# Performance work log

Measured on AMD Instinct MI355X. Metric: run time of the kernel, lower is better.

Reference implementation:

```python
import jax, jax.numpy as jnp
import numpy as np

B, Q, N, E, D, H, EDIM = 64, 50, 32, 64, 128, 4, 8
NEG = -1e30

def _ln(x, g, b, eps=1e-5):
    mu = x.mean(-1, keepdims=True)
    var = ((x - mu) ** 2).mean(-1, keepdims=True)
    return (x - mu) / jnp.sqrt(var + eps) * g + b

def setup_inputs():
    key = jax.random.key(0)
    ks = jax.random.split(key, 12)
    s = 1.0 / np.sqrt(D)
    return {
        "query_embeddings": jax.random.normal(ks[0], (B, Q, N, D), jnp.float32),
        "query_maskings": jnp.ones((B, Q, N), jnp.int32),
        "edge_indexes": jax.random.randint(ks[1], (B, Q, 2, E), 0, N, dtype=jnp.int32),
        "edge_weights": jax.random.randint(ks[2], (B, Q, E), 0, 2, dtype=jnp.int32),
        "edge_maskings": jnp.ones((B, Q, E), jnp.int32),
        "ln1_g": jnp.ones((D,), jnp.float32),
        "ln1_b": jnp.zeros((D,), jnp.float32),
        "emb_table": jax.random.normal(ks[3], (2, EDIM), jnp.float32),
        "Wl": jax.random.normal(ks[4], (D, H * D), jnp.float32) * s,
        "bl": jnp.zeros((H * D,), jnp.float32),
        "Wr": jax.random.normal(ks[5], (D, H * D), jnp.float32) * s,
        "br": jnp.zeros((H * D,), jnp.float32),
        "We": jax.random.normal(ks[6], (EDIM, H * D), jnp.float32) / np.sqrt(EDIM),
        "att": jax.random.normal(ks[7], (H, D), jnp.float32) * s,
        "gat_b": jnp.zeros((D,), jnp.float32),
        "W1": jax.random.normal(ks[8], (D, D), jnp.float32) * s,
        "b1": jnp.zeros((D,), jnp.float32),
        "W2": jax.random.normal(ks[9], (D, D), jnp.float32) * s,
        "b2": jnp.zeros((D,), jnp.float32),
        "ln2_g": jnp.ones((D,), jnp.float32),
        "ln2_b": jnp.zeros((D,), jnp.float32),
    }

def _gat_graph(x, src, dst, eemb, emask, Wl, bl, Wr, br, We, att, gat_b):
    # GATv2Conv, heads=H, concat=False, add_self_loops=True (fill_value='mean')
    # x [N,D]; src,dst [E]; eemb [E,EDIM]; emask [E] float
    xl = (x @ Wl + bl).reshape(N, H, D)
    xr = (x @ Wr + br).reshape(N, H, D)
    # self-loop edge_attr = mean of incoming (valid) edge attrs per target node
    ecnt = jax.ops.segment_sum(emask, dst, num_segments=N)
    loop_attr = jax.ops.segment_sum(eemb * emask[:, None], dst, num_segments=N) / jnp.maximum(ecnt, 1.0)[:, None]
    e = (eemb @ We).reshape(E, H, D)
    le = (loop_attr @ We).reshape(N, H, D)
    z = jax.nn.leaky_relu(xl[src] + xr[dst] + e, 0.2)
    logits = jnp.where(emask[:, None] > 0, jnp.einsum('ehd,hd->eh', z, att), NEG)
    zs = jax.nn.leaky_relu(xl + xr + le, 0.2)  # self-loop terms
    logits_s = jnp.einsum('nhd,hd->nh', zs, att)
    # segment softmax over incoming edges + self loop
    m = jnp.maximum(jax.ops.segment_max(logits, dst, num_segments=N), logits_s)  # [N,H]
    exp_e = jnp.where(emask[:, None] > 0, jnp.exp(logits - m[dst]), 0.0)
    exp_s = jnp.exp(logits_s - m)
    denom = jax.ops.segment_sum(exp_e, dst, num_segments=N) + exp_s
    agg = jax.ops.segment_sum(xl[src] * (exp_e / denom[dst])[:, :, None], dst, num_segments=N)
    agg = agg + xl * (exp_s / denom)[:, :, None]
    return agg.mean(axis=1) + gat_b  # concat=False -> mean over heads, + bias

def _forward(query_embeddings, ln1_g, ln1_b, emb_table, Wl, bl, Wr, br, We, att, gat_b,
             W1, b1, W2, b2, ln2_g, ln2_b,
             query_maskings, edge_indexes, edge_weights, edge_maskings):
    x = _ln(query_embeddings, ln1_g, ln1_b)                 # [B,Q,N,D]
    nmask = query_maskings.astype(jnp.float32)              # [B,Q,N]
    emask = edge_maskings.astype(jnp.float32)               # [B,Q,E]
    valid = ((query_maskings.sum(-1) > 0) & (edge_maskings.sum(-1) > 0)).astype(jnp.float32)  # [B,Q]
    eemb = emb_table[edge_weights]                          # [B,Q,E,EDIM]
    G = B * Q
    xf = x.reshape(G, N, D)
    srcf = edge_indexes[:, :, 0, :].reshape(G, E)
    dstf = edge_indexes[:, :, 1, :].reshape(G, E)
    eembf = eemb.reshape(G, E, EDIM)
    emaskf = emask.reshape(G, E)
    gat = jax.vmap(_gat_graph, in_axes=(0, 0, 0, 0, 0) + (None,) * 7)
    gout = gat(xf, srcf, dstf, eembf, emaskf, Wl, bl, Wr, br, We, att, gat_b)  # [G,N,D]
    h = jax.nn.leaky_relu(gout @ W1 + b1, 0.01) @ W2 + b2   # FFN (dropout = eval no-op)
    nmf = nmask.reshape(G, N)
    pooled = (h * nmf[:, :, None]).sum(1) / jnp.maximum(nmf.sum(1), 1.0)[:, None]  # global mean pool
    res = pooled.reshape(B, Q, D) * valid[:, :, None]       # invalid queries stay zero
    return _ln(res, ln2_g, ln2_b)

def reference(query_embeddings, query_maskings, edge_indexes, edge_weights, edge_maskings,
              ln1_g, ln1_b, emb_table, Wl, bl, Wr, br, We, att, gat_b,
              W1, b1, W2, b2, ln2_g, ln2_b):
    return _forward(query_embeddings, ln1_g, ln1_b, emb_table, Wl, bl, Wr, br, We, att, gat_b,
                    W1, b1, W2, b2, ln2_g, ln2_b,
                    query_maskings, edge_indexes, edge_weights, edge_maskings)
```

## Files before the change

### kernel.cpp

```cpp
#include <hip/hip_runtime.h>
#include <math.h>

#define B_ 64
#define Q_ 50
#define N_ 32
#define E_ 64
#define D_ 128
#define H_ 4
#define EDIM_ 8
#define G_ (B_*Q_)

#define WLP_OFF 0
#define WRP_OFF 131072
#define W1P_OFF 262144
#define W2P_OFF 294912
#define EW_OFF  327680

typedef __attribute__((ext_vector_type(8))) short short8;
typedef __attribute__((ext_vector_type(4))) float f32x4;
typedef __attribute__((ext_vector_type(4))) unsigned uint4e;
typedef __attribute__((ext_vector_type(2))) unsigned uint2e;
typedef __attribute__((ext_vector_type(2))) _Float16 half2e;
typedef __attribute__((ext_vector_type(2))) __fp16 fp16v2;
typedef unsigned short ushort_t;
typedef unsigned long long u64;

__device__ __forceinline__ int boff(int r, int d) {
  return (r << 7) + ((d & 0x78) ^ ((r & 7) << 3)) + (d & 7);
}

__device__ __forceinline__ ushort_t f2b(float f) {
  unsigned u = __float_as_uint(f);
  u += 0x7fffu + ((u >> 16) & 1u);
  return (ushort_t)(u >> 16);
}
__device__ __forceinline__ float b2f(ushort_t u) {
  return __uint_as_float(((unsigned)u) << 16);
}
__device__ __forceinline__ unsigned cvtpk(float lo, float hi) {
  unsigned r;
  asm("v_cvt_pk_bf16_f32 %0, %1, %2" : "=v"(r) : "v"(lo), "v"(hi));
  return r;
}
__device__ __forceinline__ unsigned pkrtz(float lo, float hi) {
  union { fp16v2 h; unsigned u; } x;
  x.h = __builtin_amdgcn_cvt_pkrtz(lo, hi);
  return x.u;
}
__device__ __forceinline__ half2e u2h(unsigned u) {
  union { unsigned u; half2e h; } x; x.u = u; return x.h;
}
__device__ __forceinline__ float leakyf(float v, float s) {
  return fmaxf(v, s * v);
}
__device__ __forceinline__ void syncb() {
  asm volatile("s_waitcnt lgkmcnt(0)" ::: "memory");
  __builtin_amdgcn_s_barrier();
  asm volatile("" ::: "memory");
}

__global__ __launch_bounds__(256)
void pack_weights(const float* __restrict__ Wl, const float* __restrict__ Wr,
                  const float* __restrict__ W1, const float* __restrict__ W2,
                  const float* __restrict__ embT, const float* __restrict__ We,
                  unsigned char* __restrict__ ws)
{
  const int i = blockIdx.x * 256 + threadIdx.x;
  ushort_t* wlp = (ushort_t*)(ws + WLP_OFF);
  ushort_t* wrp = (ushort_t*)(ws + WRP_OFF);
  ushort_t* w1p = (ushort_t*)(ws + W1P_OFF);
  ushort_t* w2p = (ushort_t*)(ws + W2P_OFF);
  float* ew = (float*)(ws + EW_OFF);
  if (i < 65536) {
    const int kk = i & 31, n = (i >> 5) & 127, q = (i >> 12) & 3, h = i >> 14;
    wlp[i] = f2b(Wl[(q * 32 + kk) * (H_ * D_) + h * D_ + n]);
    wrp[i] = f2b(Wr[(q * 32 + kk) * (H_ * D_) + h * D_ + n]);
  } else if (i < 65536 + 16384) {
    const int j = i - 65536;
    const int kk = j & 31, n = (j >> 5) & 127, q = j >> 12;
    w1p[j] = f2b(W1[(q * 32 + kk) * D_ + n]);
    w2p[j] = f2b(W2[(q * 32 + kk) * D_ + n]);
  } else if (i < 65536 + 16384 + 1024) {
    const int j = i - 65536 - 16384;
    const int w = j >> 9, hd = j & 511;
    float a = 0.f;
#pragma unroll
    for (int k = 0; k < EDIM_; ++k) a = fmaf(embT[w * EDIM_ + k], We[k * (H_ * D_) + hd], a);
    ew[j] = a;
  }
}

template <bool F16OUT, bool LEAKY>
__device__ __forceinline__ void gemm_e(const short8 aF[2][4], const ushort_t* __restrict__ Bp,
                                       const float* __restrict__ bias, float slope,
                                       ushort_t* __restrict__ dst, int lane, int nq)
{
#pragma unroll
  for (int nt = 0; nt < 2; ++nt) {
    const int colw = nq * 32 + nt * 16 + (lane & 15);
    const int oc0 = nq * 32 + nt * 16 + ((lane >> 4) << 2);
    const float4 bb = *(const float4*)&bias[oc0];
    f32x4 acc0 = {0.f, 0.f, 0.f, 0.f}, acc1 = {0.f, 0.f, 0.f, 0.f};
#pragma unroll
    for (int q = 0; q < 4; ++q) {
      const short8 b = *(const short8*)&Bp[((q << 7) + colw) * 32 + ((lane >> 4) << 3)];
      acc0 = __builtin_amdgcn_mfma_f32_16x16x32_bf16(b, aF[0][q], acc0, 0, 0, 0);
      acc1 = __builtin_amdgcn_mfma_f32_16x16x32_bf16(b, aF[1][q], acc1, 0, 0, 0);
    }
#pragma unroll
    for (int cc = 0; cc < 2; ++cc) {
      const f32x4 a = cc ? acc1 : acc0;
      const int node = cc * 16 + (lane & 15);
      float v0 = a[0] + bb.x, v1 = a[1] + bb.y, v2 = a[2] + bb.z, v3 = a[3] + bb.w;
      if (LEAKY) {
        v0 = leakyf(v0, slope); v1 = leakyf(v1, slope);
        v2 = leakyf(v2, slope); v3 = leakyf(v3, slope);
      }
      uint2e o;
      if (F16OUT) {
        o.x = pkrtz(v0, v1);
        o.y = pkrtz(v2, v3);
      } else {
        o.x = cvtpk(v0, v1);
        o.y = cvtpk(v2, v3);
      }
      *(uint2e*)&dst[boff(node, oc0)] = o;
    }
  }
}

__global__ __launch_bounds__(256, 4)
void gat_main(const unsigned char* __restrict__ ws,
              const float* __restrict__ qe,
              const float* __restrict__ ln1g, const float* __restrict__ ln1b,
              const int* __restrict__ qmask, const int* __restrict__ eidx,
              const int* __restrict__ ewt, const int* __restrict__ emsk,
              const float* __restrict__ bl, const float* __restrict__ br,
              const float* __restrict__ att, const float* __restrict__ gatb,
              const float* __restrict__ b1, const float* __restrict__ b2,
              const float* __restrict__ ln2g, const float* __restrict__ ln2b,
              float* __restrict__ out)
{
  const int g = blockIdx.x, t = threadIdx.x;
  const int lane = t & 63, wave = t >> 6;

  __shared__ __align__(16) ushort_t sX[N_ * D_];
  __shared__ __align__(16) ushort_t sXl[N_ * D_];
  __shared__ __align__(16) ushort_t sXr[N_ * D_];
  __shared__ u64 sInc[N_];
  __shared__ int sSrc[E_], sDst[E_], sWt[E_];
  __shared__ float sEm[E_], sNm[N_], sC0[N_], sC1[N_];
  __shared__ float sValid, sNmSum;

  ushort_t* sEW  = sX;
  ushort_t* sAtt = sX + 1024;
  float* sExpE = (float*)(sX + 1536);
  float* sExpS = (float*)(sX + 1664);
  float* sPool = (float*)(sX + 1728);

  const ushort_t* wlp = (const ushort_t*)(ws + WLP_OFF);
  const ushort_t* wrp = (const ushort_t*)(ws + WRP_OFF);
  const ushort_t* w1p = (const ushort_t*)(ws + W1P_OFF);
  const ushort_t* w2p = (const ushort_t*)(ws + W2P_OFF);

  {
    const int r = t >> 3, d0 = (t & 7) << 4;
    const f32x4* src4 = (const f32x4*)(qe + ((size_t)g * N_ + r) * D_ + d0);
    f32x4 v4[4];
#pragma unroll
    for (int p = 0; p < 4; ++p) v4[p] = __builtin_nontemporal_load(src4 + p);
    const float* v = (const float*)v4;
    float s = 0.f, ss = 0.f;
#pragma unroll
    for (int i = 0; i < 16; ++i) { float x = v[i]; s += x; ss += x * x; }
#pragma unroll
    for (int m = 1; m < 8; m <<= 1) { s += __shfl_xor(s, m); ss += __shfl_xor(ss, m); }
    const float mu = s * (1.f / 128.f);
    const float inv = rsqrtf(ss * (1.f / 128.f) - mu * mu + 1e-5f);
    const f32x4* gg = (const f32x4*)&ln1g[d0];
    const f32x4* bb = (const f32x4*)&ln1b[d0];
    float o[16];
#pragma unroll
    for (int p = 0; p < 4; ++p) {
      const f32x4 g4 = gg[p], b4 = bb[p];
#pragma unroll
      for (int k = 0; k < 4; ++k)
        o[p * 4 + k] = (v[p * 4 + k] - mu) * inv * g4[k] + b4[k];
    }
    uint4e w0, w1;
    w0.x = cvtpk(o[0], o[1]);  w0.y = cvtpk(o[2], o[3]);
    w0.z = cvtpk(o[4], o[5]);  w0.w = cvtpk(o[6], o[7]);
    w1.x = cvtpk(o[8], o[9]);  w1.y = cvtpk(o[10], o[11]);
    w1.z = cvtpk(o[12], o[13]); w1.w = cvtpk(o[14], o[15]);
    *(uint4e*)&sX[boff(r, d0)] = w0;
    *(uint4e*)&sX[boff(r, d0 + 8)] = w1;
  }
  if (t < E_) {
    sSrc[t] = eidx[(size_t)g * 2 * E_ + t];
    sDst[t] = eidx[(size_t)g * 2 * E_ + E_ + t];
    sWt[t] = ewt[(size_t)g * E_ + t];
    sEm[t] = (float)emsk[(size_t)g * E_ + t];
  } else if (t < 96) {
    sNm[t - 64] = (float)qmask[(size_t)g * N_ + (t - 64)];
  }
  syncb();

  short8 aF[2][4];
#pragma unroll
  for (int c = 0; c < 2; ++c)
#pragma unroll
    for (int q = 0; q < 4; ++q)
      aF[c][q] = *(const short8*)&sX[boff(c * 16 + (lane & 15), q * 32 + ((lane >> 4) << 3))];

  {
    const int dl = sDst[lane];
    const float eml = sEm[lane];
    const int wtl = sWt[lane];
    const bool val = eml > 0.f;
    const u64 wt0m = __ballot(wtl == 0);
#pragma unroll
    for (int k = 0; k < 8; ++k) {
      const int n = wave * 8 + k;
      const u64 inc = __ballot(val && dl == n);
      if (lane == k) {
        sInc[n] = inc;
        const float cnt = (float)__popcll(inc);
        const float c0 = (float)__popcll(inc & wt0m);
        const float rinv = 1.f / fmaxf(cnt, 1.f);
        sC0[n] = c0 * rinv;
        sC1[n] = (cnt - c0) * rinv;
      }
    }
    if (wave == 3) {
      float nmv = (lane < 32) ? sNm[lane] : 0.f;
      float emv = eml;
#pragma unroll
      for (int m = 1; m < 64; m <<= 1) { nmv += __shfl_xor(nmv, m); emv += __shfl_xor(emv, m); }
      if (lane == 0) {
        sNmSum = nmv;
        sValid = (nmv > 0.f && emv > 0.f) ? 1.f : 0.f;
      }
    }
  }
  syncb();

  {
    const float* ewg = (const float*)(ws + EW_OFF);
    const f32x4 e4 = *(const f32x4*)&ewg[t << 2];
    uint2e p;
    p.x = pkrtz(e4[0], e4[1]);
    p.y = pkrtz(e4[2], e4[3]);
    *(uint2e*)&sEW[t << 2] = p;
    if (t < 128) {
      const f32x4 a4 = *(const f32x4*)&att[t << 2];
      uint2e q;
      q.x = pkrtz(a4[0], a4[1]);
      q.y = pkrtz(a4[2], a4[3]);
      *(uint2e*)&sAtt[t << 2] = q;
    }
  }

  const half2e pslope = {(_Float16)0.2f, (_Float16)0.2f};
  half2e accA[4] = {}, accB[4] = {};

  for (int h = 0; h < H_; ++h) {
    gemm_e<true, false>(aF, wlp + h * 16384, bl + h * D_, 0.f, sXl, lane, wave);
    gemm_e<true, false>(aF, wrp + h * 16384, br + h * D_, 0.f, sXr, lane, wave);
    syncb();
    {
      const int e = t >> 2, qu = t & 3;
      const int sn = sSrc[e], dn = sDst[e];
      const int ewb = (sWt[e] << 9) + (h << 7);
      float dx = 0.f, dy = 0.f;
#pragma unroll
      for (int ch = 0; ch < 4; ++ch) {
        const int dd = qu * 32 + ch * 8;
        const uint4e xlu = *(const uint4e*)&sXl[boff(sn, dd)];
        const uint4e xru = *(const uint4e*)&sXr[boff(dn, dd)];
        const uint4e ewu = *(const uint4e*)&sEW[ewb + dd];
        const uint4e atu = *(const uint4e*)&sAtt[(h << 7) + dd];
#pragma unroll
        for (int k = 0; k < 4; ++k) {
          half2e z = u2h(xlu[k]) + u2h(xru[k]) + u2h(ewu[k]);
          z = __builtin_elementwise_max(z, z * pslope);
          if (k & 1) dy = __builtin_amdgcn_fdot2(z, u2h(atu[k]), dy, false);
          else       dx = __builtin_amdgcn_fdot2(z, u2h(atu[k]), dx, false);
        }
      }
      float dot = dx + dy;
      dot += __shfl_xor(dot, 1);
      dot += __shfl_xor(dot, 2);
      const float ex = (sEm[e] > 0.f) ? __expf(dot) : 0.f;
      if (qu == 0) sExpE[e] = ex;
    }
    {
      const int n = t >> 3, l8 = t & 7;
      const half2e c02 = {(_Float16)sC0[n], (_Float16)sC0[n]};
      const half2e c12 = {(_Float16)sC1[n], (_Float16)sC1[n]};
      float dx = 0.f, dy = 0.f;
#pragma unroll
      for (int ch = 0; ch < 2; ++ch) {
        const int dd = (l8 << 4) + ch * 8;
        const uint4e xlu = *(const uint4e*)&sXl[boff(n, dd)];
        const uint4e xru = *(const uint4e*)&sXr[boff(n, dd)];
        const uint4e e0u = *(const uint4e*)&sEW[(h << 7) + dd];
        const uint4e e1u = *(const uint4e*)&sEW[512 + (h << 7) + dd];
        const uint4e atu = *(const uint4e*)&sAtt[(h << 7) + dd];
#pragma unroll
        for (int k = 0; k < 4; ++k) {
          half2e lw = u2h(e0u[k]) * c02 + u2h(e1u[k]) * c12;
          half2e z = u2h(xlu[k]) + u2h(xru[k]) + lw;
          z = __builtin_elementwise_max(z, z * pslope);
          if (k & 1) dy = __builtin_amdgcn_fdot2(z, u2h(atu[k]), dy, false);
          else       dx = __builtin_amdgcn_fdot2(z, u2h(atu[k]), dx, false);
        }
      }
      float dot = dx + dy;
      dot += __shfl_xor(dot, 1);
      dot += __shfl_xor(dot, 2);
      dot += __shfl_xor(dot, 4);
      if (l8 == 0) sExpS[n] = __expf(dot);
    }
    syncb();
    {
      const int n = t >> 3, l8 = t & 7, db = l8 << 4;
      const float es = sExpS[n];
      const u64 mb = sInc[n];
      float den = es;
      u64 m2 = mb;
      while (m2) { const int e = __builtin_ctzll(m2); m2 &= m2 - 1; den += sExpE[e]; }
      const float rd = 0.25f / den;
      m2 = mb;
      while (m2) {
        const int e = __builtin_ctzll(m2); m2 &= m2 - 1;
        const _Float16 wh = (_Float16)(rd * sExpE[e]);
        const half2e w2 = {wh, wh};
        const int sn = sSrc[e];
        const uint4e a0 = *(const uint4e*)&sXl[boff(sn, db)];
        const uint4e a1 = *(const uint4e*)&sXl[boff(sn, db + 8)];
#pragma unroll
        for (int k = 0; k < 4; ++k) {
          accA[k] = u2h(a0[k]) * w2 + accA[k];
          accB[k] = u2h(a1[k]) * w2 + accB[k];
        }
      }
      const _Float16 wsh = (_Float16)(rd * es);
      const half2e ws2 = {wsh, wsh};
      const uint4e s0 = *(const uint4e*)&sXl[boff(n, db)];
      const uint4e s1 = *(const uint4e*)&sXl[boff(n, db + 8)];
#pragma unroll
      for (int k = 0; k < 4; ++k) {
        accA[k] = u2h(s0[k]) * ws2 + accA[k];
        accB[k] = u2h(s1[k]) * ws2 + accB[k];
      }
    }
    syncb();
  }

  {
    const int n = t >> 3, l8 = t & 7, db = l8 << 4;
    const float4 g0 = *(const float4*)&gatb[db];
    const float4 g1 = *(const float4*)&gatb[db + 4];
    const float4 g2 = *(const float4*)&gatb[db + 8];
    const float4 g3 = *(const float4*)&gatb[db + 12];
    const float gv[16] = {g0.x, g0.y, g0.z, g0.w, g1.x, g1.y, g1.z, g1.w,
                          g2.x, g2.y, g2.z, g2.w, g3.x, g3.y, g3.z, g3.w};
    uint4e o0, o1;
    unsigned* po0 = (unsigned*)&o0;
    unsigned* po1 = (unsigned*)&o1;
#pragma unroll
    for (int k = 0; k < 4; ++k) {
      po0[k] = cvtpk((float)accA[k].x + gv[2 * k], (float)accA[k].y + gv[2 * k + 1]);
      po1[k] = cvtpk((float)accB[k].x + gv[8 + 2 * k], (float)accB[k].y + gv[8 + 2 * k + 1]);
    }
    *(uint4e*)&sX[boff(n, db)] = o0;
    *(uint4e*)&sX[boff(n, db + 8)] = o1;
  }
  syncb();

  {
    short8 aG[2][4];
#pragma unroll
    for (int c = 0; c < 2; ++c)
#pragma unroll
      for (int q = 0; q < 4; ++q)
        aG[c][q] = *(const short8*)&sX[boff(c * 16 + (lane & 15), q * 32 + ((lane >> 4) << 3))];
    gemm_e<false, true>(aG, w1p, b1, 0.01f, sXl, lane, wave);
    syncb();
#pragma unroll
    for (int c = 0; c < 2; ++c)
#pragma unroll
      for (int q = 0; q < 4; ++q)
        aG[c][q] = *(const short8*)&sXl[boff(c * 16 + (lane & 15), q * 32 + ((lane >> 4) << 3))];
    gemm_e<false, false>(aG, w2p, b2, 0.f, sXr, lane, wave);
  }
  syncb();

  if (t < D_) {
    float acc = 0.f;
    for (int n = 0; n < N_; ++n) acc = fmaf(b2f(sXr[boff(n, t)]), sNm[n], acc);
    sPool[t] = acc * (1.f / fmaxf(sNmSum, 1.f)) * sValid;
  }
  syncb();
  if (t < 64) {
    const float v0 = sPool[t], v1 = sPool[t + 64];
    float s = v0 + v1, ss = v0 * v0 + v1 * v1;
#pragma unroll
    for (int m = 1; m < 64; m <<= 1) { s += __shfl_xor(s, m); ss += __shfl_xor(ss, m); }
    const float mu = s * (1.f / 128.f);
    const float inv = rsqrtf(ss * (1.f / 128.f) - mu * mu + 1e-5f);
    float* op = out + (size_t)g * D_;
    __builtin_nontemporal_store((v0 - mu) * inv * ln2g[t] + ln2b[t], op + t);
    __builtin_nontemporal_store((v1 - mu) * inv * ln2g[t + 64] + ln2b[t + 64], op + t + 64);
  }
}

extern "C" void kernel_launch(void* const* d_in, const int* in_sizes, int n_in,
                              void* d_out, int out_size, void* d_ws, size_t ws_size,
                              hipStream_t stream) {
  (void)in_sizes; (void)n_in; (void)out_size; (void)ws_size;
  const float* qe   = (const float*)d_in[0];
  const int*   qm   = (const int*)d_in[1];
  const int*   ei   = (const int*)d_in[2];
  const int*   ew   = (const int*)d_in[3];
  const int*   em   = (const int*)d_in[4];
  const float* ln1g = (const float*)d_in[5];
  const float* ln1b = (const float*)d_in[6];
  const float* embT = (const float*)d_in[7];
  const float* Wl   = (const float*)d_in[8];
  const float* bl   = (const float*)d_in[9];
  const float* Wr   = (const float*)d_in[10];
  const float* br   = (const float*)d_in[11];
  const float* We   = (const float*)d_in[12];
  const float* att  = (const float*)d_in[13];
  const float* gatb = (const float*)d_in[14];
  const float* W1   = (const float*)d_in[15];
  const float* b1   = (const float*)d_in[16];
  const float* W2   = (const float*)d_in[17];
  const float* b2   = (const float*)d_in[18];
  const float* ln2g = (const float*)d_in[19];
  const float* ln2b = (const float*)d_in[20];
  float* out = (float*)d_out;
  unsigned char* ws = (unsigned char*)d_ws;

  pack_weights<<<dim3(324), dim3(256), 0, stream>>>(Wl, Wr, W1, W2, embT, We, ws);
  gat_main<<<dim3(G_), dim3(256), 0, stream>>>(ws, qe, ln1g, ln1b, qm, ei, ew, em,
                                               bl, br, att, gatb, b1, b2, ln2g, ln2b, out);
}
```

Baseline: 127.1 us.

## Process two attention heads per pass with four LDS projection buffers

Shared memory now holds four 32x128 bf16 projection tiles, so the Wl/Wr GEMMs for two heads are computed back to back and the edge-score, self-loop and aggregation phases handle both heads in one pass. This halves the number of barrier-separated head iterations and shares index and mask loads across two heads. The edge-weight, attention and scratch arrays get their own buffers instead of aliasing sX, and the LDS swizzle now XORs with 4 row bits instead of 3. LDS use per block grows to roughly 32KB+, which may lower occupancy under the 4-blocks launch bound, and register pressure rises.

```diff
diff --git a/kernel.cpp b/kernel.cpp
--- a/kernel.cpp
+++ b/kernel.cpp
@@ -26,7 +26,7 @@
 typedef unsigned long long u64;
 
 __device__ __forceinline__ int boff(int r, int d) {
-  return (r << 7) + ((d & 0x78) ^ ((r & 7) << 3)) + (d & 7);
+  return (r << 7) + ((d & 0x78) ^ ((r & 15) << 3)) + (d & 7);
 }
 
 __device__ __forceinline__ ushort_t f2b(float f) {
@@ -144,19 +144,17 @@
   const int g = blockIdx.x, t = threadIdx.x;
   const int lane = t & 63, wave = t >> 6;
 
-  __shared__ __align__(16) ushort_t sX[N_ * D_];
-  __shared__ __align__(16) ushort_t sXl[N_ * D_];
-  __shared__ __align__(16) ushort_t sXr[N_ * D_];
+  __shared__ __align__(16) ushort_t sT[4 * N_ * D_];
+  __shared__ __align__(16) ushort_t sEW[1024];
+  __shared__ __align__(16) ushort_t sAtt[512];
+  __shared__ float sExpE[2][E_];
+  __shared__ float sExpS[2][N_];
+  __shared__ float sPool[D_];
   __shared__ u64 sInc[N_];
   __shared__ int sSrc[E_], sDst[E_], sWt[E_];
   __shared__ float sEm[E_], sNm[N_], sC0[N_], sC1[N_];
   __shared__ float sValid, sNmSum;
-
-  ushort_t* sEW  = sX;
-  ushort_t* sAtt = sX + 1024;
-  float* sExpE = (float*)(sX + 1536);
-  float* sExpS = (float*)(sX + 1664);
-  float* sPool = (float*)(sX + 1728);
+#define T(i) (sT + (i) * (N_ * D_))
 
   const ushort_t* wlp = (const ushort_t*)(ws + WLP_OFF);
   const ushort_t* wrp = (const ushort_t*)(ws + WRP_OFF);
@@ -192,58 +190,9 @@
     w0.z = cvtpk(o[4], o[5]);  w0.w = cvtpk(o[6], o[7]);
     w1.x = cvtpk(o[8], o[9]);  w1.y = cvtpk(o[10], o[11]);
     w1.z = cvtpk(o[12], o[13]); w1.w = cvtpk(o[14], o[15]);
-    *(uint4e*)&sX[boff(r, d0)] = w0;
-    *(uint4e*)&sX[boff(r, d0 + 8)] = w1;
-  }
-  if (t < E_) {
-    sSrc[t] = eidx[(size_t)g * 2 * E_ + t];
-    sDst[t] = eidx[(size_t)g * 2 * E_ + E_ + t];
-    sWt[t] = ewt[(size_t)g * E_ + t];
-    sEm[t] = (float)emsk[(size_t)g * E_ + t];
-  } else if (t < 96) {
-    sNm[t - 64] = (float)qmask[(size_t)g * N_ + (t - 64)];
-  }
-  syncb();
-
-  short8 aF[2][4];
-#pragma unroll
-  for (int c = 0; c < 2; ++c)
-#pragma unroll
-    for (int q = 0; q < 4; ++q)
-      aF[c][q] = *(const short8*)&sX[boff(c * 16 + (lane & 15), q * 32 + ((lane >> 4) << 3))];
-
-  {
-    const int dl = sDst[lane];
-    const float eml = sEm[lane];
-    const int wtl = sWt[lane];
-    const bool val = eml > 0.f;
-    const u64 wt0m = __ballot(wtl == 0);
-#pragma unroll
-    for (int k = 0; k < 8; ++k) {
-      const int n = wave * 8 + k;
-      const u64 inc = __ballot(val && dl == n);
-      if (lane == k) {
-        sInc[n] = inc;
-        const float cnt = (float)__popcll(inc);
-        const float c0 = (float)__popcll(inc & wt0m);
-        const float rinv = 1.f / fmaxf(cnt, 1.f);
-        sC0[n] = c0 * rinv;
-        sC1[n] = (cnt - c0) * rinv;
-      }
-    }
-    if (wave == 3) {
-      float nmv = (lane < 32) ? sNm[lane] : 0.f;
-      float emv = eml;
-#pragma unroll
-      for (int m = 1; m < 64; m <<= 1) { nmv += __shfl_xor(nmv, m); emv += __shfl_xor(emv, m); }
-      if (lane == 0) {
-        sNmSum = nmv;
-        sValid = (nmv > 0.f && emv > 0.f) ? 1.f : 0.f;
-      }
-    }
-  }
-  syncb();
-
+    *(uint4e*)&T(0)[boff(r, d0)] = w0;
+    *(uint4e*)&T(0)[boff(r, d0 + 8)] = w1;
+  }
   {
     const float* ewg = (const float*)(ws + EW_OFF);
     const f32x4 e4 = *(const f32x4*)&ewg[t << 2];
@@ -259,102 +208,213 @@
       *(uint2e*)&sAtt[t << 2] = q;
     }
   }
+  if (t < E_) {
+    sSrc[t] = eidx[(size_t)g * 2 * E_ + t];
+    sDst[t] = eidx[(size_t)g * 2 * E_ + E_ + t];
+    sWt[t] = ewt[(size_t)g * E_ + t];
+    sEm[t] = (float)emsk[(size_t)g * E_ + t];
+  } else if (t < 96) {
+    sNm[t - 64] = (float)qmask[(size_t)g * N_ + (t - 64)];
+  }
+  syncb();
+
+  short8 aF[2][4];
+#pragma unroll
+  for (int c = 0; c < 2; ++c)
+#pragma unroll
+    for (int q = 0; q < 4; ++q)
+      aF[c][q] = *(const short8*)&T(0)[boff(c * 16 + (lane & 15), q * 32 + ((lane >> 4) << 3))];
+  {
+    const int dl = sDst[lane];
+    const float eml = sEm[lane];
+    const int wtl = sWt[lane];
+    const bool val = eml > 0.f;
+    const u64 wt0m = __ballot(wtl == 0);
+#pragma unroll
+    for (int k = 0; k < 8; ++k) {
+      const int n = wave * 8 + k;
+      const u64 inc = __ballot(val && dl == n);
+      if (lane == k) {
+        sInc[n] = inc;
+        const float cnt = (float)__popcll(inc);
+        const float c0 = (float)__popcll(inc & wt0m);
+        const float rinv = 1.f / fmaxf(cnt, 1.f);
+        sC0[n] = c0 * rinv;
+        sC1[n] = (cnt - c0) * rinv;
+      }
+    }
+    if (wave == 3) {
+      float nmv = (lane < 32) ? sNm[lane] : 0.f;
+      float emv = eml;
+#pragma unroll
+      for (int m = 1; m < 64; m <<= 1) { nmv += __shfl_xor(nmv, m); emv += __shfl_xor(emv, m); }
+      if (lane == 0) {
+        sNmSum = nmv;
+        sValid = (nmv > 0.f && emv > 0.f) ? 1.f : 0.f;
+      }
+    }
+  }
+  syncb();
+
+  gemm_e<true, false>(aF, wlp, bl, 0.f, T(0), lane, wave);
+  gemm_e<true, false>(aF, wrp, br, 0.f, T(1), lane, wave);
+  gemm_e<true, false>(aF, wlp + 16384, bl + D_, 0.f, T(2), lane, wave);
+  gemm_e<true, false>(aF, wrp + 16384, br + D_, 0.f, T(3), lane, wave);
+  syncb();
 
   const half2e pslope = {(_Float16)0.2f, (_Float16)0.2f};
   half2e accA[4] = {}, accB[4] = {};
 
-  for (int h = 0; h < H_; ++h) {
-    gemm_e<true, false>(aF, wlp + h * 16384, bl + h * D_, 0.f, sXl, lane, wave);
-    gemm_e<true, false>(aF, wrp + h * 16384, br + h * D_, 0.f, sXr, lane, wave);
-    syncb();
+#pragma unroll
+  for (int it = 0; it < 2; ++it) {
+    const int hA = (it * 2) << 7, hB = (it * 2 + 1) << 7;
     {
       const int e = t >> 2, qu = t & 3;
       const int sn = sSrc[e], dn = sDst[e];
-      const int ewb = (sWt[e] << 9) + (h << 7);
-      float dx = 0.f, dy = 0.f;
+      const int wb = sWt[e] << 9;
+      float dA0 = 0.f, dA1 = 0.f, dB0 = 0.f, dB1 = 0.f;
 #pragma unroll
       for (int ch = 0; ch < 4; ++ch) {
         const int dd = qu * 32 + ch * 8;
-        const uint4e xlu = *(const uint4e*)&sXl[boff(sn, dd)];
-        const uint4e xru = *(const uint4e*)&sXr[boff(dn, dd)];
-        const uint4e ewu = *(const uint4e*)&sEW[ewb + dd];
-        const uint4e atu = *(const uint4e*)&sAtt[(h << 7) + dd];
+        const int ol = boff(sn, dd), od = boff(dn, dd);
+        const uint4e xlA = *(const uint4e*)&T(0)[ol];
+        const uint4e xrA = *(const uint4e*)&T(1)[od];
+        const uint4e xlB = *(const uint4e*)&T(2)[ol];
+        const uint4e xrB = *(const uint4e*)&T(3)[od];
+        const uint4e ewA = *(const uint4e*)&sEW[wb + hA + dd];
+        const uint4e ewB = *(const uint4e*)&sEW[wb + hB + dd];
+        const uint4e atA = *(const uint4e*)&sAtt[hA + dd];
+        const uint4e atB = *(const uint4e*)&sAtt[hB + dd];
 #pragma unroll
         for (int k = 0; k < 4; ++k) {
-          half2e z = u2h(xlu[k]) + u2h(xru[k]) + u2h(ewu[k]);
-          z = __builtin_elementwise_max(z, z * pslope);
-          if (k & 1) dy = __builtin_amdgcn_fdot2(z, u2h(atu[k]), dy, false);
-          else       dx = __builtin_amdgcn_fdot2(z, u2h(atu[k]), dx, false);
+          half2e zA = u2h(xlA[k]) + u2h(xrA[k]) + u2h(ewA[k]);
+          zA = __builtin_elementwise_max(zA, zA * pslope);
+          half2e zB = u2h(xlB[k]) + u2h(xrB[k]) + u2h(ewB[k]);
+          zB = __builtin_elementwise_max(zB, zB * pslope);
+          if (k & 1) {
+            dA1 = __builtin_amdgcn_fdot2(zA, u2h(atA[k]), dA1, false);
+            dB1 = __builtin_amdgcn_fdot2(zB, u2h(atB[k]), dB1, false);
+          } else {
+            dA0 = __builtin_amdgcn_fdot2(zA, u2h(atA[k]), dA0, false);
+            dB0 = __builtin_amdgcn_fdot2(zB, u2h(atB[k]), dB0, false);
+          }
         }
       }
-      float dot = dx + dy;
-      dot += __shfl_xor(dot, 1);
-      dot += __shfl_xor(dot, 2);
-      const float ex = (sEm[e] > 0.f) ? __expf(dot) : 0.f;
-      if (qu == 0) sExpE[e] = ex;
+      float dotA = dA0 + dA1, dotB = dB0 + dB1;
+      dotA += __shfl_xor(dotA, 1);
+      dotA += __shfl_xor(dotA, 2);
+      dotB += __shfl_xor(dotB, 1);
+      dotB += __shfl_xor(dotB, 2);
+      const bool ve = sEm[e] > 0.f;
+      if (qu == 0) {
+        sExpE[0][e] = ve ? __expf(dotA) : 0.f;
+        sExpE[1][e] = ve ? __expf(dotB) : 0.f;
+      }
     }
     {
       const int n = t >> 3, l8 = t & 7;
       const half2e c02 = {(_Float16)sC0[n], (_Float16)sC0[n]};
       const half2e c12 = {(_Float16)sC1[n], (_Float16)sC1[n]};
-      float dx = 0.f, dy = 0.f;
+      float dA0 = 0.f, dA1 = 0.f, dB0 = 0.f, dB1 = 0.f;
 #pragma unroll
       for (int ch = 0; ch < 2; ++ch) {
         const int dd = (l8 << 4) + ch * 8;
-        const uint4e xlu = *(const uint4e*)&sXl[boff(n, dd)];
-        const uint4e xru = *(const uint4e*)&sXr[boff(n, dd)];
-        const uint4e e0u = *(const uint4e*)&sEW[(h << 7) + dd];
-        const uint4e e1u = *(const uint4e*)&sEW[512 + (h << 7) + dd];
-        const uint4e atu = *(const uint4e*)&sAtt[(h << 7) + dd];
+        const int on = boff(n, dd);
+        const uint4e xlA = *(const uint4e*)&T(0)[on];
+        const uint4e xrA = *(const uint4e*)&T(1)[on];
+        const uint4e xlB = *(const uint4e*)&T(2)[on];
+        const uint4e xrB = *(const uint4e*)&T(3)[on];
+        const uint4e e0A = *(const uint4e*)&sEW[hA + dd];
+        const uint4e e1A = *(const uint4e*)&sEW[512 + hA + dd];
+        const uint4e e0B = *(const uint4e*)&sEW[hB + dd];
+        const uint4e e1B = *(const uint4e*)&sEW[512 + hB + dd];
+        const uint4e atA = *(const uint4e*)&sAtt[hA + dd];
+        const uint4e atB = *(const uint4e*)&sAtt[hB + dd];
 #pragma unroll
         for (int k = 0; k < 4; ++k) {
-          half2e lw = u2h(e0u[k]) * c02 + u2h(e1u[k]) * c12;
-          half2e z = u2h(xlu[k]) + u2h(xru[k]) + lw;
-          z = __builtin_elementwise_max(z, z * pslope);
-          if (k & 1) dy = __builtin_amdgcn_fdot2(z, u2h(atu[k]), dy, false);
-          else       dx = __builtin_amdgcn_fdot2(z, u2h(atu[k]), dx, false);
+          half2e lwA = u2h(e0A[k]) * c02 + u2h(e1A[k]) * c12;
+          half2e zA = u2h(xlA[k]) + u2h(xrA[k]) + lwA;
+          zA = __builtin_elementwise_max(zA, zA * pslope);
+          half2e lwB = u2h(e0B[k]) * c02 + u2h(e1B[k]) * c12;
+          half2e zB = u2h(xlB[k]) + u2h(xrB[k]) + lwB;
+          zB = __builtin_elementwise_max(zB, zB * pslope);
+          if (k & 1) {
+            dA1 = __builtin_amdgcn_fdot2(zA, u2h(atA[k]), dA1, false);
+            dB1 = __builtin_amdgcn_fdot2(zB, u2h(atB[k]), dB1, false);
+          } else {
+            dA0 = __builtin_amdgcn_fdot2(zA, u2h(atA[k]), dA0, false);
+            dB0 = __builtin_amdgcn_fdot2(zB, u2h(atB[k]), dB0, false);
+          }
         }
       }
-      float dot = dx + dy;
-      dot += __shfl_xor(dot, 1);
-      dot += __shfl_xor(dot, 2);
-      dot += __shfl_xor(dot, 4);
-      if (l8 == 0) sExpS[n] = __expf(dot);
+      float dotA = dA0 + dA1, dotB = dB0 + dB1;
+      dotA += __shfl_xor(dotA, 1);
+      dotA += __shfl_xor(dotA, 2);
+      dotA += __shfl_xor(dotA, 4);
+      dotB += __shfl_xor(dotB, 1);
+      dotB += __shfl_xor(dotB, 2);
+      dotB += __shfl_xor(dotB, 4);
+      if (l8 == 0) {
+        sExpS[0][n] = __expf(dotA);
+        sExpS[1][n] = __expf(dotB);
+      }
     }
     syncb();
     {
       const int n = t >> 3, l8 = t & 7, db = l8 << 4;
-      const float es = sExpS[n];
+      const float esA = sExpS[0][n], esB = sExpS[1][n];
       const u64 mb = sInc[n];
-      float den = es;
+      float denA = esA, denB = esB;
       u64 m2 = mb;
-      while (m2) { const int e = __builtin_ctzll(m2); m2 &= m2 - 1; den += sExpE[e]; }
-      const float rd = 0.25f / den;
+      while (m2) {
+        const int e = __builtin_ctzll(m2); m2 &= m2 - 1;
+        denA += sExpE[0][e];
+        denB += sExpE[1][e];
+      }
+      const float rdA = 0.25f / denA, rdB = 0.25f / denB;
       m2 = mb;
       while (m2) {
         const int e = __builtin_ctzll(m2); m2 &= m2 - 1;
-        const _Float16 wh = (_Float16)(rd * sExpE[e]);
-        const half2e w2 = {wh, wh};
         const int sn = sSrc[e];
-        const uint4e a0 = *(const uint4e*)&sXl[boff(sn, db)];
-        const uint4e a1 = *(const uint4e*)&sXl[boff(sn, db + 8)];
+        const _Float16 wA = (_Float16)(rdA * sExpE[0][e]);
+        const _Float16 wB = (_Float16)(rdB * sExpE[1][e]);
+        const half2e wA2 = {wA, wA}, wB2 = {wB, wB};
+        const int o0 = boff(sn, db), o1 = boff(sn, db + 8);
+        const uint4e aA0 = *(const uint4e*)&T(0)[o0];
+        const uint4e aA1 = *(const uint4e*)&T(0)[o1];
+        const uint4e aB0 = *(const uint4e*)&T(2)[o0];
+        const uint4e aB1 = *(const uint4e*)&T(2)[o1];
 #pragma unroll
         for (int k = 0; k < 4; ++k) {
-          accA[k] = u2h(a0[k]) * w2 + accA[k];
-          accB[k] = u2h(a1[k]) * w2 + accB[k];
+          accA[k] = u2h(aA0[k]) * wA2 + accA[k];
+          accB[k] = u2h(aA1[k]) * wA2 + accB[k];
+          accA[k] = u2h(aB0[k]) * wB2 + accA[k];
+          accB[k] = u2h(aB1[k]) * wB2 + accB[k];
         }
       }
-      const _Float16 wsh = (_Float16)(rd * es);
-      const half2e ws2 = {wsh, wsh};
-      const uint4e s0 = *(const uint4e*)&sXl[boff(n, db)];
-      const uint4e s1 = *(const uint4e*)&sXl[boff(n, db + 8)];
+      const _Float16 wsA = (_Float16)(rdA * esA), wsB = (_Float16)(rdB * esB);
+      const half2e wsA2 = {wsA, wsA}, wsB2 = {wsB, wsB};
+      const int o0 = boff(n, db), o1 = boff(n, db + 8);
+      const uint4e sA0 = *(const uint4e*)&T(0)[o0];
+      const uint4e sA1 = *(const uint4e*)&T(0)[o1];
+      const uint4e sB0 = *(const uint4e*)&T(2)[o0];
+      const uint4e sB1 = *(const uint4e*)&T(2)[o1];
 #pragma unroll
       for (int k = 0; k < 4; ++k) {
-        accA[k] = u2h(s0[k]) * ws2 + accA[k];
-        accB[k] = u2h(s1[k]) * ws2 + accB[k];
+        accA[k] = u2h(sA0[k]) * wsA2 + accA[k];
+        accB[k] = u2h(sA1[k]) * wsA2 + accB[k];
+        accA[k] = u2h(sB0[k]) * wsB2 + accA[k];
+        accB[k] = u2h(sB1[k]) * wsB2 + accB[k];
       }
     }
     syncb();
+    if (it == 0) {
+      gemm_e<true, false>(aF, wlp + 2 * 16384, bl + 2 * D_, 0.f, T(0), lane, wave);
+      gemm_e<true, false>(aF, wrp + 2 * 16384, br + 2 * D_, 0.f, T(1), lane, wave);
+      gemm_e<true, false>(aF, wlp + 3 * 16384, bl + 3 * D_, 0.f, T(2), lane, wave);
+      gemm_e<true, false>(aF, wrp + 3 * 16384, br + 3 * D_, 0.f, T(3), lane, wave);
+      syncb();
+    }
   }
 
   {
@@ -373,8 +433,8 @@
       po0[k] = cvtpk((float)accA[k].x + gv[2 * k], (float)accA[k].y + gv[2 * k + 1]);
       po1[k] = cvtpk((float)accB[k].x + gv[8 + 2 * k], (float)accB[k].y + gv[8 + 2 * k + 1]);
     }
-    *(uint4e*)&sX[boff(n, db)] = o0;
-    *(uint4e*)&sX[boff(n, db + 8)] = o1;
+    *(uint4e*)&T(0)[boff(n, db)] = o0;
+    *(uint4e*)&T(0)[boff(n, db + 8)] = o1;
   }
   syncb();
 
@@ -384,21 +444,21 @@
     for (int c = 0; c < 2; ++c)
 #pragma unroll
       for (int q = 0; q < 4; ++q)
-        aG[c][q] = *(const short8*)&sX[boff(c * 16 + (lane & 15), q * 32 + ((lane >> 4) << 3))];
-    gemm_e<false, true>(aG, w1p, b1, 0.01f, sXl, lane, wave);
+        aG[c][q] = *(const short8*)&T(0)[boff(c * 16 + (lane & 15), q * 32 + ((lane >> 4) << 3))];
+    gemm_e<false, true>(aG, w1p, b1, 0.01f, T(1), lane, wave);
     syncb();
 #pragma unroll
     for (int c = 0; c < 2; ++c)
 #pragma unroll
       for (int q = 0; q < 4; ++q)
-        aG[c][q] = *(const short8*)&sXl[boff(c * 16 + (lane & 15), q * 32 + ((lane >> 4) << 3))];
-    gemm_e<false, false>(aG, w2p, b2, 0.f, sXr, lane, wave);
+        aG[c][q] = *(const short8*)&T(1)[boff(c * 16 + (lane & 15), q * 32 + ((lane >> 4) << 3))];
+    gemm_e<false, false>(aG, w2p, b2, 0.f, T(2), lane, wave);
   }
   syncb();
 
   if (t < D_) {
     float acc = 0.f;
-    for (int n = 0; n < N_; ++n) acc = fmaf(b2f(sXr[boff(n, t)]), sNm[n], acc);
+    for (int n = 0; n < N_; ++n) acc = fmaf(b2f(T(2)[boff(n, t)]), sNm[n], acc);
     sPool[t] = acc * (1.f / fmaxf(sNmSum, 1.f)) * sValid;
   }
   syncb();
@@ -413,6 +473,7 @@
     __builtin_nontemporal_store((v0 - mu) * inv * ln2g[t] + ln2b[t], op + t);
     __builtin_nontemporal_store((v1 - mu) * inv * ln2g[t + 64] + ln2b[t + 64], op + t + 64);
   }
+#undef T
 }
 
 extern "C" void kernel_launch(void* const* d_in, const int* in_sizes, int n_in,
```

Result: no change. 127.2 us (+0.1%).
